# Kernel tuning notes

Measured on AMD Instinct MI355X. Metric: run time of the kernel, lower is better.

The kernel has to match this reference:

```python
import jax, jax.numpy as jnp
import numpy as np

N_PTS = 131072
IN_CH = 63
IN_CH_VIEWS = 27
WIDTH = 256
NUM_HEADS = 4
SCALE = 0.05


def setup_inputs() -> dict:
    key = jax.random.key(0)
    ks = jax.random.split(key, 12)
    H, W = NUM_HEADS, WIDTH
    inp = {
        'x': jax.random.normal(ks[0], (N_PTS, IN_CH + IN_CH_VIEWS), jnp.float32),
        'head_idx': jax.random.randint(ks[1], (N_PTS,), 0, NUM_HEADS),
        # shared trunk: layer0 63->256, layers1..3 256->256 (no skip before split_at=4)
        'W0': jax.random.normal(ks[2], (IN_CH, W), jnp.float32) * SCALE,
        'b0': jnp.zeros((W,), jnp.float32),
        'Ws': jax.random.normal(ks[3], (3, W, W), jnp.float32) * SCALE,
        'bs': jnp.zeros((3, W), jnp.float32),
        # per-head tails: g=4 in skips -> (W+63)->W, then g=5..7 W->W
        'tW0': jax.random.normal(ks[4], (H, W + IN_CH, W), jnp.float32) * SCALE,
        'tb0': jnp.zeros((H, W), jnp.float32),
        'tWs': jax.random.normal(ks[5], (H, 3, W, W), jnp.float32) * SCALE,
        'tbs': jnp.zeros((H, 3, W), jnp.float32),
        # per-head viewdirs output heads
        'featW': jax.random.normal(ks[6], (H, W, W), jnp.float32) * SCALE,
        'featb': jnp.zeros((H, W), jnp.float32),
        'alphaW': jax.random.normal(ks[7], (H, W, 1), jnp.float32) * SCALE,
        'alphab': jnp.zeros((H, 1), jnp.float32),
        'viewsW': jax.random.normal(ks[8], (H, IN_CH_VIEWS + W, W // 2), jnp.float32) * SCALE,
        'viewsb': jnp.zeros((H, W // 2), jnp.float32),
        'rgbW': jax.random.normal(ks[9], (H, W // 2, 3), jnp.float32) * SCALE,
        'rgbb': jnp.zeros((H, 3), jnp.float32),
    }
    return inp


def reference(x, head_idx, W0, b0, Ws, bs, tW0, tb0, tWs, tbs,
              featW, featb, alphaW, alphab, viewsW, viewsb, rgbW, rgbb):
    input_pts = x[:, :IN_CH]          # [N, 63]
    input_views = x[:, IN_CH:]        # [N, 27]

    # shared trunk (layers 0..3, no skip hits in this range)
    h = jax.nn.relu(input_pts @ W0 + b0)
    for i in range(Ws.shape[0]):
        h = jax.nn.relu(h @ Ws[i] + bs[i])

    # per-head tails, computed densely for ALL heads (as in the original)
    # first tail layer g=4 is a skip layer: concat input_pts
    ht = jnp.concatenate([input_pts, h], axis=-1)          # [N, 319]
    ha = jax.nn.relu(jnp.einsum('nf,hfo->nho', ht, tW0) + tb0[None])  # [N, H, 256]
    for j in range(tWs.shape[1]):
        ha = jax.nn.relu(jnp.einsum('nho,hop->nhp', ha, tWs[:, j]) + tbs[None, :, j])

    # per-head viewdir output heads
    alpha = jnp.einsum('nho,hop->nhp', ha, alphaW) + alphab[None]     # [N, H, 1]
    feat = jnp.einsum('nho,hop->nhp', ha, featW) + featb[None]        # [N, H, 256]
    views_b = jnp.broadcast_to(input_views[:, None, :], (x.shape[0], feat.shape[1], IN_CH_VIEWS))
    hv = jnp.concatenate([feat, views_b], axis=-1)                    # [N, H, 283]
    hv = jax.nn.relu(jnp.einsum('nho,hop->nhp', hv, viewsW) + viewsb[None])
    rgb = jnp.einsum('nho,hop->nhp', hv, rgbW) + rgbb[None]           # [N, H, 3]

    outs = jnp.concatenate([rgb, alpha], axis=-1)                     # [N, H, 4]
    sel = jnp.take_along_axis(outs, head_idx[:, None, None], axis=1)[:, 0]  # [N, 4]
    return sel
```

## Files before the change

### kernel.cpp

```cpp
#include <hip/hip_runtime.h>

#define N_PTS 131072
#define TILE 64
#define THREADS 256
#define REGION 40960

typedef __bf16 bf16;
typedef __bf16 bf16x8 __attribute__((ext_vector_type(8)));
typedef float f32x4 __attribute__((ext_vector_type(4)));

#define WS_PERM_OFF   256
#define WS_WPACK_OFF  (256 + 4 * REGION * 4)
#define OFF_W0     0
#define OFF_WS     16384
#define OFF_TW0    212992
#define OFF_TWS    540672
#define OFF_FEATW  1327104
#define OFF_VIEWSW 1589248
#define TOTAL_PACK 1736704

#define H_BASE     0
#define PTS_BASE   32768
#define VIEWS_BASE 40960
#define PIDX_BASE  45056
#define RING_BASE  46080
#define LDS_BYTES  78848

__device__ __forceinline__ unsigned swz(unsigned base, unsigned row, unsigned rowstride,
                                        unsigned kbyte) {
  return (base + row * rowstride + kbyte) ^ ((row & 7u) << 4);
}

__device__ __forceinline__ void gload_lds16(const bf16* g, char* l) {
  __builtin_amdgcn_global_load_lds(
      (const __attribute__((address_space(1))) void*)g,
      (__attribute__((address_space(3))) void*)l, 16, 0, 0);
}

template <int N>
__device__ __forceinline__ void wait_vm() {
  asm volatile("s_waitcnt vmcnt(%0)" ::"n"(N) : "memory");
}

__global__ void k_pack(const float* __restrict__ W0, const float* __restrict__ Ws,
                       const float* __restrict__ tW0, const float* __restrict__ tWs,
                       const float* __restrict__ featW, const float* __restrict__ viewsW,
                       bf16* __restrict__ out, const int* __restrict__ head,
                       int* __restrict__ ctrl, int* __restrict__ perm) {
  int gid = blockIdx.x * blockDim.x + threadIdx.x;
  if (gid < N_PTS) {
    int h = head[gid];
    int lane = threadIdx.x & 63;
    #pragma unroll
    for (int hh = 0; hh < 4; ++hh) {
      unsigned long long m = __ballot(h == hh);
      if (m == 0ull) continue;
      int leader = __builtin_ctzll(m);
      int base = 0;
      if (lane == leader) base = atomicAdd(&ctrl[16 + hh], __popcll(m));
      base = __shfl(base, leader);
      if (h == hh) {
        int rank = __popcll(m & ((1ull << lane) - 1ull));
        perm[hh * REGION + base + rank] = gid;
      }
    }
  }

  for (int idx = gid; idx < TOTAL_PACK; idx += gridDim.x * blockDim.x) {
    float v; int dst;
    if (idx < 16384) {
      int k = idx >> 8, o = idx & 255;
      v = (k < 63) ? W0[k * 256 + o] : 0.f;
      dst = OFF_W0 + o * 64 + k;
    } else if (idx < 212992) {
      int i = idx - 16384; int l = i >> 16, r = i & 65535, k = r >> 8, o = r & 255;
      v = Ws[i];
      dst = OFF_WS + l * 65536 + o * 256 + k;
    } else if (idx < 540672) {
      int i = idx - 212992; int h = i / 81920, r = i % 81920, k = r >> 8, o = r & 255;
      v = (k < 63) ? tW0[(h * 319 + k) * 256 + o]
                   : (k == 63 ? 0.f : tW0[(h * 319 + k - 1) * 256 + o]);
      dst = OFF_TW0 + h * 81920 + o * 320 + k;
    } else if (idx < 1327104) {
      int i = idx - 540672; int hj = i >> 16, r = i & 65535, k = r >> 8, o = r & 255;
      v = tWs[i];
      dst = OFF_TWS + hj * 65536 + o * 256 + k;
    } else if (idx < 1589248) {
      int i = idx - 1327104; int h = i >> 16, r = i & 65535, k = r >> 8, o = r & 255;
      v = featW[i];
      dst = OFF_FEATW + h * 65536 + o * 256 + k;
    } else {
      int i = idx - 1589248; int h = i / 36864, r = i % 36864, k = r >> 7, o = r & 127;
      v = (k < 283) ? viewsW[(h * 283 + k) * 128 + o] : 0.f;
      dst = OFF_VIEWSW + h * 36864 + o * 288 + k;
    }
    out[dst] = (bf16)v;
  }
}

template <int NF, bool RELU, int PKC, int LKC, bool PTS_FIRST, int AUXB, int AUXSTR,
          int NEXTNF>
__device__ __forceinline__ void mfma_layer(char* lds, const bf16* __restrict__ Wt,
                                           int wK, const float* __restrict__ bias,
                                           const bf16* __restrict__ nextWt, int nextwK,
                                           int lane, int wave) {
  const int l15 = lane & 15, l4 = lane >> 4;
  constexpr int KC = PKC + LKC;
  f32x4 acc[4][NF];
  #pragma unroll
  for (int m = 0; m < 4; ++m)
    #pragma unroll
    for (int n = 0; n < NF; ++n) acc[m][n] = (f32x4){0.f, 0.f, 0.f, 0.f};

  const int c0 = wave * (NF * 16);
  const int wbase = RING_BASE + wave * 8192;

  float bv[NF];
  #pragma unroll
  for (int n = 0; n < NF; ++n) bv[n] = bias[c0 + n * 16 + l15];

  const int breg = wbase + l15 * 64 + ((l4 ^ ((l15 >> 1) & 3)) << 4);

  unsigned acur = (unsigned)(l15 * 512 + l4 * 16);
  const unsigned axor = (l15 & 7u) << 4;

  const bf16* gsrc[NF];
  #pragma unroll
  for (int s = 0; s < NF; ++s) {
    int op = s * 16 + (lane >> 2);
    int j = lane & 3;
    gsrc[s] = Wt + (c0 + op) * wK + ((j ^ ((op >> 1) & 3)) << 3) + 32;
  }

  #pragma unroll
  for (int kc = 0; kc < KC; ++kc) {
    if (kc + 1 < KC) {
      #pragma unroll
      for (int s = 0; s < NF; ++s) {
        gload_lds16(gsrc[s], lds + wbase + ((kc + 1) & 1) * 4096 + s * 1024);
        gsrc[s] += 32;
      }
      wait_vm<NF>();
    } else if constexpr (NEXTNF > 0) {
      #pragma unroll
      for (int s = 0; s < NEXTNF; ++s) {
        int op = s * 16 + (lane >> 2);
        int j = lane & 3;
        const bf16* g = nextWt + (wave * NEXTNF * 16 + op) * nextwK +
                        ((j ^ ((op >> 1) & 3)) << 3);
        gload_lds16(g, lds + wbase + s * 1024);
      }
      wait_vm<NEXTNF>();
    } else {
      wait_vm<0>();
    }

    bf16x8 a[4];
    if (PTS_FIRST ? (kc < PKC) : (kc >= LKC)) {
      const int kcp = PTS_FIRST ? kc : 0;
      #pragma unroll
      for (int m = 0; m < 4; ++m) {
        unsigned ad = (unsigned)(AUXB + (m * 16 + l15) * AUXSTR + kcp * 64 + l4 * 16) ^ axor;
        a[m] = *(const bf16x8*)(lds + ad);
      }
    } else {
      unsigned va = acur ^ axor;
      #pragma unroll
      for (int m = 0; m < 4; ++m) a[m] = *(const bf16x8*)(lds + va + m * 8192);
      acur += 64;
    }
    bf16x8 b[NF];
    #pragma unroll
    for (int n = 0; n < NF; ++n)
      b[n] = *(const bf16x8*)(lds + breg + (kc & 1) * 4096 + n * 1024);

    __builtin_amdgcn_s_setprio(1);
    #pragma unroll
    for (int n = 0; n < NF; ++n)
      #pragma unroll
      for (int m = 0; m < 4; ++m)
        acc[m][n] = __builtin_amdgcn_mfma_f32_16x16x32_bf16(a[m], b[n], acc[m][n], 0, 0, 0);
    __builtin_amdgcn_s_setprio(0);
  }

  __builtin_amdgcn_s_barrier();

  #pragma unroll
  for (int n = 0; n < NF; ++n) {
    int col = c0 + n * 16 + l15;
    #pragma unroll
    for (int m = 0; m < 4; ++m) {
      #pragma unroll
      for (int j = 0; j < 4; ++j) {
        float v = acc[m][n][j] + bv[n];
        if (RELU) v = fmaxf(v, 0.f);
        int row = m * 16 + l4 * 4 + j;
        *(bf16*)(lds + swz(H_BASE, row, 512, col * 2)) = (bf16)v;
      }
    }
  }
  asm volatile("s_waitcnt lgkmcnt(0)" ::: "memory");
  __builtin_amdgcn_s_barrier();
}

__global__ __launch_bounds__(THREADS, 2) void k_main(
    const float* __restrict__ x, const int* __restrict__ ctrl, const int* __restrict__ perm,
    const bf16* __restrict__ wpack,
    const float* __restrict__ b0, const float* __restrict__ bs,
    const float* __restrict__ tb0, const float* __restrict__ tbs,
    const float* __restrict__ featb, const float* __restrict__ alphaW,
    const float* __restrict__ alphab, const float* __restrict__ viewsb,
    const float* __restrict__ rgbW, const float* __restrict__ rgbb,
    float* __restrict__ outp) {
  __shared__ __attribute__((aligned(16))) char lds[LDS_BYTES];
  int* pidxl = (int*)(lds + PIDX_BASE);

  const int tid = threadIdx.x;
  const int lane = tid & 63, wave = tid >> 6;
  const int l15 = lane & 15, l4 = lane >> 4;

  const int hh = blockIdx.x / (REGION / TILE);
  const int start = (blockIdx.x % (REGION / TILE)) * TILE;
  const int cnt = ctrl[16 + hh];
  if (start >= cnt) return;
  const int nv = min(TILE, cnt - start);
  const int permbase = hh * REGION + start;

  if (tid < TILE) pidxl[tid] = (tid < nv) ? perm[permbase + tid] : 0;
  __syncthreads();

  for (int i = tid; i < TILE * 64; i += THREADS) {
    int row = i >> 6, c = i & 63;
    float v = (row < nv && c < 63) ? x[pidxl[row] * 90 + c] : 0.f;
    *(bf16*)(lds + ((PTS_BASE + row * 128 + c * 2) ^ ((row & 7u) << 4))) = (bf16)v;
  }
  for (int i = tid; i < TILE * 32; i += THREADS) {
    int row = i >> 5, c = i & 31;
    float v = (row < nv && c < 27) ? x[pidxl[row] * 90 + 63 + c] : 0.f;
    *(bf16*)(lds + ((VIEWS_BASE + row * 64 + c * 2) ^ ((row & 7u) << 4))) = (bf16)v;
  }

  const bf16* W0p    = wpack + OFF_W0;
  const bf16* Wsp    = wpack + OFF_WS;
  const bf16* tW0p   = wpack + OFF_TW0 + hh * 81920;
  const bf16* tWsp   = wpack + OFF_TWS + hh * 3 * 65536;
  const bf16* featWp = wpack + OFF_FEATW + hh * 65536;
  const bf16* viewsWp= wpack + OFF_VIEWSW + hh * 36864;

  {
    const int wbase = RING_BASE + wave * 8192;
    const int c0 = wave * 64;
    #pragma unroll
    for (int s = 0; s < 4; ++s) {
      int op = s * 16 + (lane >> 2);
      int j = lane & 3;
      gload_lds16(W0p + (c0 + op) * 64 + ((j ^ ((op >> 1) & 3)) << 3),
                  lds + wbase + s * 1024);
    }
  }
  asm volatile("s_waitcnt lgkmcnt(0)" ::: "memory");
  __builtin_amdgcn_s_barrier();

  mfma_layer<4, true, 2, 0, true,  PTS_BASE, 128, 4>(lds, W0p, 64, b0, Wsp, 256, lane, wave);
  mfma_layer<4, true, 0, 8, false, 0, 0,      4>(lds, Wsp,          256, bs,       Wsp + 65536,  256, lane, wave);
  mfma_layer<4, true, 0, 8, false, 0, 0,      4>(lds, Wsp + 65536,  256, bs + 256, Wsp + 131072, 256, lane, wave);
  mfma_layer<4, true, 0, 8, false, 0, 0,      4>(lds, Wsp + 131072, 256, bs + 512, tW0p,         320, lane, wave);
  mfma_layer<4, true, 2, 8, true,  PTS_BASE, 128, 4>(lds, tW0p, 320, tb0 + hh * 256, tWsp, 256, lane, wave);

  mfma_layer<4, true, 0, 8, false, 0, 0, 4>(lds, tWsp,          256, tbs + hh * 768,       tWsp + 65536,  256, lane, wave);
  mfma_layer<4, true, 0, 8, false, 0, 0, 4>(lds, tWsp + 65536,  256, tbs + hh * 768 + 256, tWsp + 131072, 256, lane, wave);
  mfma_layer<4, true, 0, 8, false, 0, 0, 4>(lds, tWsp + 131072, 256, tbs + hh * 768 + 512, featWp,        256, lane, wave);

  float my_alpha;
  {
    int p = wave * 16 + l15;
    int kq = lane >> 4;
    const float* aW = alphaW + hh * 256;
    float s = 0.f;
    for (int i = 0; i < 8; ++i) {
      int k = kq * 64 + i * 8;
      bf16x8 hv8 = *(const bf16x8*)(lds + swz(H_BASE, p, 512, k * 2));
      #pragma unroll
      for (int j = 0; j < 8; ++j) s += (float)hv8[j] * aW[k + j];
    }
    s += __shfl_xor(s, 16);
    s += __shfl_xor(s, 32);
    my_alpha = s + alphab[hh];
  }

  mfma_layer<4, false, 0, 8, false, 0, 0, 2>(lds, featWp, 256, featb + hh * 256, viewsWp, 288, lane, wave);
  mfma_layer<2, true, 1, 8, false, VIEWS_BASE, 64, 0>(lds, viewsWp, 288, viewsb + hh * 128,
                                                      nullptr, 0, lane, wave);

  {
    int p = wave * 16 + l15;
    int kq = lane >> 4;
    const float* rW = rgbW + hh * 128 * 3;
    float r0 = 0.f, r1 = 0.f, r2 = 0.f;
    for (int i = 0; i < 4; ++i) {
      int k = kq * 32 + i * 8;
      bf16x8 hv8 = *(const bf16x8*)(lds + swz(H_BASE, p, 512, k * 2));
      #pragma unroll
      for (int j = 0; j < 8; ++j) {
        float hvf = (float)hv8[j];
        r0 += hvf * rW[(k + j) * 3 + 0];
        r1 += hvf * rW[(k + j) * 3 + 1];
        r2 += hvf * rW[(k + j) * 3 + 2];
      }
    }
    r0 += __shfl_xor(r0, 16); r0 += __shfl_xor(r0, 32);
    r1 += __shfl_xor(r1, 16); r1 += __shfl_xor(r1, 32);
    r2 += __shfl_xor(r2, 16); r2 += __shfl_xor(r2, 32);
    if (kq == 0 && p < nv) {
      int pt = pidxl[p];
      float4 o = make_float4(r0 + rgbb[hh * 3 + 0], r1 + rgbb[hh * 3 + 1],
                             r2 + rgbb[hh * 3 + 2], my_alpha);
      *(float4*)(outp + pt * 4) = o;
    }
  }
}

extern "C" void kernel_launch(void* const* d_in, const int* in_sizes, int n_in,
                              void* d_out, int out_size, void* d_ws, size_t ws_size,
                              hipStream_t stream) {
  const float* x      = (const float*)d_in[0];
  const int*   head   = (const int*)d_in[1];
  const float* W0     = (const float*)d_in[2];
  const float* b0     = (const float*)d_in[3];
  const float* Ws     = (const float*)d_in[4];
  const float* bs     = (const float*)d_in[5];
  const float* tW0    = (const float*)d_in[6];
  const float* tb0    = (const float*)d_in[7];
  const float* tWs    = (const float*)d_in[8];
  const float* tbs    = (const float*)d_in[9];
  const float* featW  = (const float*)d_in[10];
  const float* featb  = (const float*)d_in[11];
  const float* alphaW = (const float*)d_in[12];
  const float* alphab = (const float*)d_in[13];
  const float* viewsW = (const float*)d_in[14];
  const float* viewsb = (const float*)d_in[15];
  const float* rgbW   = (const float*)d_in[16];
  const float* rgbb   = (const float*)d_in[17];

  int*  ctrl  = (int*)d_ws;
  int*  perm  = (int*)((char*)d_ws + WS_PERM_OFF);
  bf16* wpack = (bf16*)((char*)d_ws + WS_WPACK_OFF);

  hipMemsetAsync(ctrl, 0, 256, stream);
  k_pack<<<2048, 256, 0, stream>>>(W0, Ws, tW0, tWs, featW, viewsW, wpack, head, ctrl, perm);
  k_main<<<4 * (REGION / TILE), THREADS, 0, stream>>>(x, ctrl, perm, wpack,
                                                      b0, bs, tb0, tbs, featb, alphaW, alphab,
                                                      viewsb, rgbW, rgbb, (float*)d_out);
}
```

Before: 460.0 us.

## Load MFMA weight operands directly from global into registers, drop LDS ring

Replaces the per-wave LDS double-buffered weight ring (global_load_lds plus vmcnt waits) with direct global-to-register loads of B fragments, prefetched two k-steps ahead in two register buffers. The shared LDS footprint shrinks, and launch bounds rise from 2 to 3 blocks per CU to raise occupancy. This trades LDS staging for more register pressure and relies on L1/L2 to serve the weights instead of coalesced LDS staging. Global loads are now 16-byte per lane with row stride wK, which may be less coalesced.

```diff
diff --git a/kernel.cpp b/kernel.cpp
--- a/kernel.cpp
+++ b/kernel.cpp
@@ -23,23 +23,11 @@
 #define PTS_BASE   32768
 #define VIEWS_BASE 40960
 #define PIDX_BASE  45056
-#define RING_BASE  46080
-#define LDS_BYTES  78848
+#define LDS_BYTES  45312
 
 __device__ __forceinline__ unsigned swz(unsigned base, unsigned row, unsigned rowstride,
                                         unsigned kbyte) {
   return (base + row * rowstride + kbyte) ^ ((row & 7u) << 4);
-}
-
-__device__ __forceinline__ void gload_lds16(const bf16* g, char* l) {
-  __builtin_amdgcn_global_load_lds(
-      (const __attribute__((address_space(1))) void*)g,
-      (__attribute__((address_space(3))) void*)l, 16, 0, 0);
-}
-
-template <int N>
-__device__ __forceinline__ void wait_vm() {
-  asm volatile("s_waitcnt vmcnt(%0)" ::"n"(N) : "memory");
 }
 
 __global__ void k_pack(const float* __restrict__ W0, const float* __restrict__ Ws,
@@ -98,11 +86,41 @@
   }
 }
 
-template <int NF, bool RELU, int PKC, int LKC, bool PTS_FIRST, int AUXB, int AUXSTR,
-          int NEXTNF>
+#define DOSTEP(KCV, BUF)                                                        \
+  do {                                                                          \
+    bf16x8 a[4];                                                                \
+    if (PTS_FIRST ? ((KCV) < PKC) : ((KCV) >= LKC)) {                           \
+      const int kcp = PTS_FIRST ? (KCV) : 0;                                    \
+      _Pragma("unroll")                                                         \
+      for (int m = 0; m < 4; ++m) {                                             \
+        unsigned ad = (unsigned)(AUXB + (m * 16 + l15) * AUXSTR + kcp * 64 +    \
+                                 l4 * 16) ^ axor;                               \
+        a[m] = *(const bf16x8*)(lds + ad);                                      \
+      }                                                                         \
+    } else {                                                                    \
+      unsigned va = acur ^ axor;                                                \
+      _Pragma("unroll")                                                         \
+      for (int m = 0; m < 4; ++m) a[m] = *(const bf16x8*)(lds + va + m * 8192); \
+      acur += 64;                                                               \
+    }                                                                           \
+    __builtin_amdgcn_s_setprio(1);                                              \
+    _Pragma("unroll")                                                           \
+    for (int n = 0; n < NF; ++n)                                                \
+      _Pragma("unroll")                                                         \
+      for (int m = 0; m < 4; ++m)                                               \
+        acc[m][n] = __builtin_amdgcn_mfma_f32_16x16x32_bf16(a[m], BUF[n],       \
+                                                            acc[m][n], 0, 0, 0);\
+    __builtin_amdgcn_s_setprio(0);                                              \
+    if ((KCV) + 2 < KC) {                                                       \
+      _Pragma("unroll")                                                         \
+      for (int n = 0; n < NF; ++n)                                              \
+        BUF[n] = *(const bf16x8*)(Wt + boff[n] + ((KCV) + 2) * 32);             \
+    }                                                                           \
+  } while (0)
+
+template <int NF, bool RELU, int PKC, int LKC, bool PTS_FIRST, int AUXB, int AUXSTR>
 __device__ __forceinline__ void mfma_layer(char* lds, const bf16* __restrict__ Wt,
                                            int wK, const float* __restrict__ bias,
-                                           const bf16* __restrict__ nextWt, int nextwK,
                                            int lane, int wave) {
   const int l15 = lane & 15, l4 = lane >> 4;
   constexpr int KC = PKC + LKC;
@@ -113,75 +131,32 @@
     for (int n = 0; n < NF; ++n) acc[m][n] = (f32x4){0.f, 0.f, 0.f, 0.f};
 
   const int c0 = wave * (NF * 16);
-  const int wbase = RING_BASE + wave * 8192;
 
   float bv[NF];
   #pragma unroll
   for (int n = 0; n < NF; ++n) bv[n] = bias[c0 + n * 16 + l15];
 
-  const int breg = wbase + l15 * 64 + ((l4 ^ ((l15 >> 1) & 3)) << 4);
+  int boff[NF];
+  #pragma unroll
+  for (int n = 0; n < NF; ++n) boff[n] = (c0 + n * 16 + l15) * wK + l4 * 8;
+
+  bf16x8 bc[NF], bn[NF];
+  #pragma unroll
+  for (int n = 0; n < NF; ++n) bc[n] = *(const bf16x8*)(Wt + boff[n]);
+  if (KC > 1) {
+    #pragma unroll
+    for (int n = 0; n < NF; ++n) bn[n] = *(const bf16x8*)(Wt + boff[n] + 32);
+  }
 
   unsigned acur = (unsigned)(l15 * 512 + l4 * 16);
   const unsigned axor = (l15 & 7u) << 4;
 
-  const bf16* gsrc[NF];
-  #pragma unroll
-  for (int s = 0; s < NF; ++s) {
-    int op = s * 16 + (lane >> 2);
-    int j = lane & 3;
-    gsrc[s] = Wt + (c0 + op) * wK + ((j ^ ((op >> 1) & 3)) << 3) + 32;
-  }
-
-  #pragma unroll
-  for (int kc = 0; kc < KC; ++kc) {
-    if (kc + 1 < KC) {
-      #pragma unroll
-      for (int s = 0; s < NF; ++s) {
-        gload_lds16(gsrc[s], lds + wbase + ((kc + 1) & 1) * 4096 + s * 1024);
-        gsrc[s] += 32;
-      }
-      wait_vm<NF>();
-    } else if constexpr (NEXTNF > 0) {
-      #pragma unroll
-      for (int s = 0; s < NEXTNF; ++s) {
-        int op = s * 16 + (lane >> 2);
-        int j = lane & 3;
-        const bf16* g = nextWt + (wave * NEXTNF * 16 + op) * nextwK +
-                        ((j ^ ((op >> 1) & 3)) << 3);
-        gload_lds16(g, lds + wbase + s * 1024);
-      }
-      wait_vm<NEXTNF>();
-    } else {
-      wait_vm<0>();
-    }
-
-    bf16x8 a[4];
-    if (PTS_FIRST ? (kc < PKC) : (kc >= LKC)) {
-      const int kcp = PTS_FIRST ? kc : 0;
-      #pragma unroll
-      for (int m = 0; m < 4; ++m) {
-        unsigned ad = (unsigned)(AUXB + (m * 16 + l15) * AUXSTR + kcp * 64 + l4 * 16) ^ axor;
-        a[m] = *(const bf16x8*)(lds + ad);
-      }
-    } else {
-      unsigned va = acur ^ axor;
-      #pragma unroll
-      for (int m = 0; m < 4; ++m) a[m] = *(const bf16x8*)(lds + va + m * 8192);
-      acur += 64;
-    }
-    bf16x8 b[NF];
-    #pragma unroll
-    for (int n = 0; n < NF; ++n)
-      b[n] = *(const bf16x8*)(lds + breg + (kc & 1) * 4096 + n * 1024);
-
-    __builtin_amdgcn_s_setprio(1);
-    #pragma unroll
-    for (int n = 0; n < NF; ++n)
-      #pragma unroll
-      for (int m = 0; m < 4; ++m)
-        acc[m][n] = __builtin_amdgcn_mfma_f32_16x16x32_bf16(a[m], b[n], acc[m][n], 0, 0, 0);
-    __builtin_amdgcn_s_setprio(0);
-  }
+  #pragma unroll 1
+  for (int kc = 0; kc + 1 < KC; kc += 2) {
+    DOSTEP(kc, bc);
+    DOSTEP(kc + 1, bn);
+  }
+  if (KC & 1) DOSTEP(KC - 1, bc);
 
   __builtin_amdgcn_s_barrier();
 
@@ -203,7 +178,7 @@
   __builtin_amdgcn_s_barrier();
 }
 
-__global__ __launch_bounds__(THREADS, 2) void k_main(
+__global__ __launch_bounds__(THREADS, 3) void k_main(
     const float* __restrict__ x, const int* __restrict__ ctrl, const int* __restrict__ perm,
     const bf16* __restrict__ wpack,
     const float* __restrict__ b0, const float* __restrict__ bs,
@@ -239,6 +214,7 @@
     float v = (row < nv && c < 27) ? x[pidxl[row] * 90 + 63 + c] : 0.f;
     *(bf16*)(lds + ((VIEWS_BASE + row * 64 + c * 2) ^ ((row & 7u) << 4))) = (bf16)v;
   }
+  __syncthreads();
 
   const bf16* W0p    = wpack + OFF_W0;
   const bf16* Wsp    = wpack + OFF_WS;
@@ -247,29 +223,15 @@
   const bf16* featWp = wpack + OFF_FEATW + hh * 65536;
   const bf16* viewsWp= wpack + OFF_VIEWSW + hh * 36864;
 
-  {
-    const int wbase = RING_BASE + wave * 8192;
-    const int c0 = wave * 64;
-    #pragma unroll
-    for (int s = 0; s < 4; ++s) {
-      int op = s * 16 + (lane >> 2);
-      int j = lane & 3;
-      gload_lds16(W0p + (c0 + op) * 64 + ((j ^ ((op >> 1) & 3)) << 3),
-                  lds + wbase + s * 1024);
-    }
-  }
-  asm volatile("s_waitcnt lgkmcnt(0)" ::: "memory");
-  __builtin_amdgcn_s_barrier();
-
-  mfma_layer<4, true, 2, 0, true,  PTS_BASE, 128, 4>(lds, W0p, 64, b0, Wsp, 256, lane, wave);
-  mfma_layer<4, true, 0, 8, false, 0, 0,      4>(lds, Wsp,          256, bs,       Wsp + 65536,  256, lane, wave);
-  mfma_layer<4, true, 0, 8, false, 0, 0,      4>(lds, Wsp + 65536,  256, bs + 256, Wsp + 131072, 256, lane, wave);
-  mfma_layer<4, true, 0, 8, false, 0, 0,      4>(lds, Wsp + 131072, 256, bs + 512, tW0p,         320, lane, wave);
-  mfma_layer<4, true, 2, 8, true,  PTS_BASE, 128, 4>(lds, tW0p, 320, tb0 + hh * 256, tWsp, 256, lane, wave);
-
-  mfma_layer<4, true, 0, 8, false, 0, 0, 4>(lds, tWsp,          256, tbs + hh * 768,       tWsp + 65536,  256, lane, wave);
-  mfma_layer<4, true, 0, 8, false, 0, 0, 4>(lds, tWsp + 65536,  256, tbs + hh * 768 + 256, tWsp + 131072, 256, lane, wave);
-  mfma_layer<4, true, 0, 8, false, 0, 0, 4>(lds, tWsp + 131072, 256, tbs + hh * 768 + 512, featWp,        256, lane, wave);
+  mfma_layer<4, true, 2, 0, true,  PTS_BASE, 128>(lds, W0p, 64, b0, lane, wave);
+  mfma_layer<4, true, 0, 8, false, 0, 0>(lds, Wsp,          256, bs,       lane, wave);
+  mfma_layer<4, true, 0, 8, false, 0, 0>(lds, Wsp + 65536,  256, bs + 256, lane, wave);
+  mfma_layer<4, true, 0, 8, false, 0, 0>(lds, Wsp + 131072, 256, bs + 512, lane, wave);
+  mfma_layer<4, true, 2, 8, true,  PTS_BASE, 128>(lds, tW0p, 320, tb0 + hh * 256, lane, wave);
+
+  mfma_layer<4, true, 0, 8, false, 0, 0>(lds, tWsp,          256, tbs + hh * 768,       lane, wave);
+  mfma_layer<4, true, 0, 8, false, 0, 0>(lds, tWsp + 65536,  256, tbs + hh * 768 + 256, lane, wave);
+  mfma_layer<4, true, 0, 8, false, 0, 0>(lds, tWsp + 131072, 256, tbs + hh * 768 + 512, lane, wave);
 
   float my_alpha;
   {
@@ -288,9 +250,9 @@
     my_alpha = s + alphab[hh];
   }
 
-  mfma_layer<4, false, 0, 8, false, 0, 0, 2>(lds, featWp, 256, featb + hh * 256, viewsWp, 288, lane, wave);
-  mfma_layer<2, true, 1, 8, false, VIEWS_BASE, 64, 0>(lds, viewsWp, 288, viewsb + hh * 128,
-                                                      nullptr, 0, lane, wave);
+  mfma_layer<4, false, 0, 8, false, 0, 0>(lds, featWp, 256, featb + hh * 256, lane, wave);
+  mfma_layer<2, true, 1, 8, false, VIEWS_BASE, 64>(lds, viewsWp, 288, viewsb + hh * 128,
+                                                   lane, wave);
 
   {
     int p = wave * 16 + l15;
```

Result: slower. 676.5 us (+47.1%).
